# Performance work log

Measured on AMD Instinct MI355X. Metric: run time of the kernel, lower is better.

Reference implementation:

```python
import jax, jax.numpy as jnp
import numpy as np

N = 512       # n_nodes (also number of per-node attention heads)
F_IN = 256    # n_feature
H = 64        # h_feature
C = 64        # n_class (must equal H for V * out broadcast)
K = 12        # top-K threshold for learned adjacency
ALPHA = 0.2   # LeakyReLU negative slope


def setup_inputs() -> dict:
    key = jax.random.key(0)
    ks = jax.random.split(key, 6)
    X = jax.random.normal(ks[0], (N, F_IN), jnp.float32)
    # stacked params of the n_nodes first-layer attention heads
    W_stack = jax.random.normal(ks[1], (N, F_IN, H), jnp.float32) * 0.05
    a_stack = jax.random.normal(ks[2], (N, 2 * H, 1), jnp.float32) * 0.05
    # output attention layer: in_Channel = h_feature * n_nodes
    W_out = jax.random.normal(ks[3], (H * N, C), jnp.float32) * 0.02
    a_out = jax.random.normal(ks[4], (2 * C, 1), jnp.float32) * 0.05
    V = jax.random.normal(ks[5], (N, H), jnp.float32) * 0.1
    return {"X": X, "W_stack": W_stack, "a_stack": a_stack,
            "W_out": W_out, "a_out": a_out, "V": V}


def gat_layer(Hx, adj, W, a):
    # Faithful to Graph_Attention_Covlayer.forward, but the O(N^2 * 2F)
    # concat tensor is algebraically collapsed: concat(Wh[i], Wh[j]) @ a
    # == (Wh @ a1)[i] + (Wh @ a2)[j], a broadcast sum.
    Wh = Hx @ W                      # (N, F)
    f = W.shape[1]
    e1 = Wh @ a[:f, 0]               # (N,)
    e2 = Wh @ a[f:, 0]               # (N,)
    S = jax.nn.leaky_relu(e1[:, None] + e2[None, :], ALPHA)  # (N, N)
    A = jax.nn.softmax(S, axis=1)    # softmax BEFORE masking, as in source
    A = jnp.where(adj > 0, A, jnp.zeros_like(A))
    out = A @ Wh                     # (N, F)
    return jax.nn.elu(out)           # concat=True -> elu


def adj_learn(V):
    A = V @ V.T                      # (N, N)
    kth = jax.lax.top_k(A.reshape(-1), K)[0][-1]
    # source: Adj = 1 where A > kth-value, else 0 (strict >)
    return jnp.where(A > kth, jnp.ones_like(A), jnp.zeros_like(A))


def reference(X, W_stack, a_stack, W_out, a_out, V):
    adj = adj_learn(V)
    # all n_nodes heads share input X and adj -> vmap over stacked params
    heads = jax.vmap(lambda W, a: gat_layer(X, adj, W, a))(W_stack, a_stack)  # (N_heads, N, H)
    # torch.cat(..., dim=1): row i = [head0_feats | head1_feats | ...]
    mid = jnp.transpose(heads, (1, 0, 2)).reshape(N, N * H)
    # dropout: eval mode -> identity
    out = gat_layer(mid, adj, W_out, a_out)  # (N, C)
    out = jax.nn.elu(V * out)
    return adj, out
```

## Files before the change

kernel.cpp:

```cpp
#include <hip/hip_runtime.h>


#define CAND_OFF 0
#define XT_OFF   12288
#define KTH_OFF  143360
#define INT_OFF  143424
#define W1_OFF   143488
#define W2_OFF   274560
#define E2P_OFF  405632
#define MIDC_OFF 1454208
#define PART_OFF 1847424

#define H_M      0
#define H_R      1
#define H_ROWS   2
#define H_ER     14
#define H_EJ     26
#define H_ECJ    38

__device__ __forceinline__ float leaky_(float x) { return fmaxf(x, 0.2f * x); }
__device__ __forceinline__ float elu_(float x)   { return x > 0.f ? x : __expf(x) - 1.f; }

__global__ __launch_bounds__(256) void k1_prep(const float* __restrict__ V,
                                               const float* __restrict__ X,
                                               const float* __restrict__ Wst,
                                               const float* __restrict__ ast,
                                               float* __restrict__ wsf,
                                               float* __restrict__ out) {
  __shared__ float vi[64];
  __shared__ float wv[48]; __shared__ int wi[48];
  __shared__ float tile[64][65];
  int b = blockIdx.x, t = threadIdx.x, l = t & 63, w = t >> 6;

  if (b < 512) {
    if (t < 64) vi[t] = V[b * 64 + t];
    __syncthreads();
    float vr0, vr1;
    {
      const float4* vj = reinterpret_cast<const float4*>(V + t * 64);
      float acc = 0.f;
      #pragma unroll
      for (int q = 0; q < 16; ++q) {
        float4 v4 = vj[q];
        acc += v4.x * vi[q*4] + v4.y * vi[q*4+1] + v4.z * vi[q*4+2] + v4.w * vi[q*4+3];
      }
      vr0 = acc;
    }
    {
      const float4* vj = reinterpret_cast<const float4*>(V + (t + 256) * 64);
      float acc = 0.f;
      #pragma unroll
      for (int q = 0; q < 16; ++q) {
        float4 v4 = vj[q];
        acc += v4.x * vi[q*4] + v4.y * vi[q*4+1] + v4.z * vi[q*4+2] + v4.w * vi[q*4+3];
      }
      vr1 = acc;
    }
    out[b * 512 + t]       = vr0;
    out[b * 512 + 256 + t] = vr1;
    if (b < 128) out[262144 + b * 256 + t] = 0.f;

    float v0 = vr0, v1 = vr1;
    int j0 = t, j1 = t + 256;
    for (int round = 0; round < 12; ++round) {
      float m; int mi;
      if (v0 >= v1) { m = v0; mi = j0; } else { m = v1; mi = j1; }
      #pragma unroll
      for (int d = 1; d < 64; d <<= 1) {
        float ov = __shfl_xor(m, d);
        int   oi = __shfl_xor(mi, d);
        if (ov > m || (ov == m && oi < mi)) { m = ov; mi = oi; }
      }
      if (l == 0) { wv[w * 12 + round] = m; wi[w * 12 + round] = mi; }
      if (mi == j0) v0 = -INFINITY;
      if (mi == j1) v1 = -INFINITY;
    }
    __syncthreads();
    if (w == 0) {
      float cv = (l < 48) ? wv[l] : -INFINITY;
      int   ci = (l < 48) ? wi[l] : 0x7FFFFFFF;
      for (int round = 0; round < 12; ++round) {
        float m = cv; int mi = ci;
        #pragma unroll
        for (int d = 1; d < 64; d <<= 1) {
          float ov = __shfl_xor(m, d);
          int   oi = __shfl_xor(mi, d);
          if (ov > m || (ov == m && oi < mi)) { m = ov; mi = oi; }
        }
        if (l == 0) {
          float2 c; c.x = m; c.y = __int_as_float(b * 512 + mi);
          *reinterpret_cast<float2*>(wsf + CAND_OFF + (b * 12 + round) * 2) = c;
        }
        if (ci == mi) cv = -INFINITY;
      }
    }
  } else if (b < 544) {
    int ti = b - 512;
    int tjj = ti & 7, tff = ti >> 3;
    int r = t >> 2, c0 = (t & 3) * 16;
    #pragma unroll
    for (int u = 0; u < 4; ++u) {
      float4 x4 = *reinterpret_cast<const float4*>(X + (tjj*64 + r)*256 + tff*64 + c0 + u*4);
      tile[c0+u*4+0][r] = x4.x; tile[c0+u*4+1][r] = x4.y;
      tile[c0+u*4+2][r] = x4.z; tile[c0+u*4+3][r] = x4.w;
    }
    __syncthreads();
    int fl = t >> 2, jc0 = (t & 3) * 16;
    #pragma unroll
    for (int u = 0; u < 4; ++u) {
      float4 o4 = make_float4(tile[fl][jc0+u*4+0], tile[fl][jc0+u*4+1],
                              tile[fl][jc0+u*4+2], tile[fl][jc0+u*4+3]);
      *reinterpret_cast<float4*>(wsf + XT_OFF + (tff*64 + fl)*512 + tjj*64 + jc0 + u*4) = o4;
    }
  } else {
    int h = b - 544;
    int kc = (t & 15) << 2;
    float4 a1q = *reinterpret_cast<const float4*>(ast + h * 128 + kc);
    float4 a2q = *reinterpret_cast<const float4*>(ast + h * 128 + 64 + kc);
    const float* Wb = Wst + h * 16384;
    float p1a[16], p2a[16];
    #pragma unroll
    for (int it = 0; it < 16; ++it) {
      float4 wq = *reinterpret_cast<const float4*>(Wb + it * 1024 + t * 4);
      p1a[it] = wq.x*a1q.x + wq.y*a1q.y + wq.z*a1q.z + wq.w*a1q.w;
      p2a[it] = wq.x*a2q.x + wq.y*a2q.y + wq.z*a2q.z + wq.w*a2q.w;
    }
    #pragma unroll
    for (int it = 0; it < 16; ++it) {
      float p1 = p1a[it], p2 = p2a[it];
      #pragma unroll
      for (int d = 1; d < 16; d <<= 1) { p1 += __shfl_xor(p1, d); p2 += __shfl_xor(p2, d); }
      if ((t & 15) == 0) {
        int f = it * 16 + (t >> 4);
        wsf[W1_OFF + h * 256 + f] = p1;
        wsf[W2_OFF + h * 256 + f] = p2;
      }
    }
  }
}

__global__ __launch_bounds__(256) void k2_e2hdr(const float* __restrict__ X,
                                                float* __restrict__ wsf) {
  __shared__ __align__(16) float As[64][68];
  __shared__ __align__(16) float Bs[64][68];
  __shared__ float redv[4]; __shared__ int redi[4];
  __shared__ float candv[12]; __shared__ int candi[12];
  __shared__ int es_s[12], rows_s[12];
  __shared__ int M_s, R_s;
  int b = blockIdx.x, t = threadIdx.x, l = t & 63, w = t >> 6;

  if (b < 256) {
    int q = b >> 6, bh = (b >> 3) & 7, bj = b & 7;
    int r = t >> 2, c0 = (t & 3) * 16;
    const float* wsrc = wsf + W2_OFF + (bh * 64 + r) * 256 + q * 64 + c0;
    const float* xsrc = X + (bj * 64 + r) * 256 + q * 64 + c0;
    #pragma unroll
    for (int u = 0; u < 4; ++u) {
      float4 a4 = *reinterpret_cast<const float4*>(wsrc + u * 4);
      float4 b4 = *reinterpret_cast<const float4*>(xsrc + u * 4);
      As[c0 + u*4 + 0][r] = a4.x; As[c0 + u*4 + 1][r] = a4.y;
      As[c0 + u*4 + 2][r] = a4.z; As[c0 + u*4 + 3][r] = a4.w;
      Bs[c0 + u*4 + 0][r] = b4.x; Bs[c0 + u*4 + 1][r] = b4.y;
      Bs[c0 + u*4 + 2][r] = b4.z; Bs[c0 + u*4 + 3][r] = b4.w;
    }
    __syncthreads();
    int th = t >> 4, tj = t & 15;
    float acc[4][4] = {};
    #pragma unroll 8
    for (int f = 0; f < 64; ++f) {
      float4 a4 = *reinterpret_cast<const float4*>(&As[f][th * 4]);
      float4 b4 = *reinterpret_cast<const float4*>(&Bs[f][tj * 4]);
      float av[4] = { a4.x, a4.y, a4.z, a4.w };
      float bv[4] = { b4.x, b4.y, b4.z, b4.w };
      #pragma unroll
      for (int i = 0; i < 4; ++i)
        #pragma unroll
        for (int j = 0; j < 4; ++j)
          acc[i][j] += av[i] * bv[j];
    }
    float* dst = wsf + E2P_OFF + q * 262144 + (bh * 64 + th * 4) * 512 + bj * 64 + tj * 4;
    #pragma unroll
    for (int i = 0; i < 4; ++i) {
      float4 o4 = make_float4(acc[i][0], acc[i][1], acc[i][2], acc[i][3]);
      *reinterpret_cast<float4*>(dst + i * 512) = o4;
    }
    return;
  }

  float v[24]; int ix[24];
  const float2* cp = reinterpret_cast<const float2*>(wsf + CAND_OFF);
  #pragma unroll
  for (int k = 0; k < 24; ++k) {
    float2 c = cp[k * 256 + t];
    v[k] = c.x; ix[k] = __float_as_int(c.y);
  }
  unsigned rm = 0;
  for (int round = 0; round < 12; ++round) {
    float m = -INFINITY; int mi = 0x7FFFFFFF; int sel = -1;
    #pragma unroll
    for (int k = 0; k < 24; ++k) {
      bool ok = ((rm >> k) & 1u) == 0u;
      bool better = ok && (v[k] > m || (v[k] == m && ix[k] < mi));
      if (better) { m = v[k]; mi = ix[k]; sel = k; }
    }
    int lmi = mi;
    #pragma unroll
    for (int d = 1; d < 64; d <<= 1) {
      float ov = __shfl_xor(m, d);
      int   oi = __shfl_xor(mi, d);
      if (ov > m || (ov == m && oi < mi)) { m = ov; mi = oi; }
    }
    if (l == 0) { redv[w] = m; redi[w] = mi; }
    __syncthreads();
    float bm = redv[0]; int bi = redi[0];
    #pragma unroll
    for (int ww = 1; ww < 4; ++ww)
      if (redv[ww] > bm || (redv[ww] == bm && redi[ww] < bi)) { bm = redv[ww]; bi = redi[ww]; }
    if (t == 0) { candv[round] = bm; candi[round] = bi; }
    if (sel >= 0 && lmi == bi) rm |= 1u << sel;
    __syncthreads();
  }
  float kv = candv[11];
  bool valid = (t < 12) && (candv[t] > kv);
  int myidx = valid ? candi[t] : 0x7FFFFFFF;
  unsigned long long vm = __ballot(valid);
  if (t < 12) {
    int rank = 0;
    #pragma unroll
    for (int q = 0; q < 12; ++q)
      if (((vm >> q) & 1ull) && candi[q] < myidx) ++rank;
    if (valid) es_s[rank] = myidx;
    if (t == 0) M_s = (int)__popcll(vm & 0xFFFull);
  }
  __syncthreads();
  int M = M_s;
  bool isent = (t < M);
  int i2 = isent ? (es_s[t] >> 9) : -1;
  int j2 = isent ? (es_s[t] & 511) : 0;
  bool isnew = isent && (t == 0 || (es_s[t - 1] >> 9) != i2);
  unsigned long long nm = __ballot(isnew);
  if (isnew) {
    int r = (int)__popcll(nm & ((1ull << t) - 1ull));
    rows_s[r] = i2;
  }
  if (t == 0) R_s = (int)__popcll(nm & 0xFFFull);
  __syncthreads();
  int R = R_s;
  int* ip = (int*)(wsf + INT_OFF);
  if (t == 0) { ip[H_M] = M; ip[H_R] = R; wsf[KTH_OFF] = kv; }
  if (t < 12) {
    ip[H_ROWS + t] = (t < R) ? rows_s[t] : 0;
    int er = 0, ecj = -1;
    if (isent) {
      er = (int)__popcll(nm & ((2ull << t) - 1ull)) - 1;
      for (int r = 0; r < R; ++r) if (rows_s[r] == j2) ecj = r;
    }
    ip[H_ER + t]  = er;
    ip[H_EJ + t]  = isent ? j2 : 0;
    ip[H_ECJ + t] = ecj;
  }
}

__global__ __launch_bounds__(256) void k3_heads(
    const float* __restrict__ X, const float* __restrict__ Wst,
    float* __restrict__ wsf, float* __restrict__ out) {
  __shared__ int   shdr[64];
  __shared__ __align__(16) float XeT[3072];
  __shared__ __align__(16) float whp[3072];
  __shared__ float w1l[256];
  __shared__ float e2s[512];
  __shared__ float whl[768];
  __shared__ float e1r[12], mr12[12], sr12[12], av12[12];
  __shared__ float redv[4], redf[48];

  int b = blockIdx.x, t = threadIdx.x, l = t & 63, w = t >> 6;
  const int* ip = (const int*)(wsf + INT_OFF);

  {
    float kv = wsf[KTH_OFF];
    float a0 = out[b * 512 + t], a1 = out[b * 512 + 256 + t];
    out[b * 512 + t]       = (a0 > kv) ? 1.f : 0.f;
    out[b * 512 + 256 + t] = (a1 > kv) ? 1.f : 0.f;
  }
  if (t < 50) shdr[t] = ip[t];
  w1l[t] = wsf[W1_OFF + b * 256 + t];
  {
    float s0 = 0.f, s1 = 0.f;
    #pragma unroll
    for (int q = 0; q < 4; ++q) {
      s0 += wsf[E2P_OFF + q * 262144 + b * 512 + t];
      s1 += wsf[E2P_OFF + q * 262144 + b * 512 + 256 + t];
    }
    e2s[t] = s0; e2s[t + 256] = s1;
  }
  __syncthreads();
  int M = shdr[H_M], R = shdr[H_R];

  #pragma unroll
  for (int m = 0; m < 12; ++m) {
    float v = 0.f;
    if (m < M) v = X[shdr[H_EJ + m] * 256 + t];
    XeT[t * 12 + m] = v;
  }
  __syncthreads();

  const float* Wb = Wst + b * 16384;
  int fg = l >> 4, kc = (l & 15) << 2;
  float wh[12][4];
  #pragma unroll
  for (int m = 0; m < 12; ++m) { wh[m][0] = wh[m][1] = wh[m][2] = wh[m][3] = 0.f; }
  #pragma unroll 4
  for (int it = 0; it < 16; ++it) {
    int f = w * 64 + it * 4 + fg;
    float4 wq = *reinterpret_cast<const float4*>(Wb + f * 64 + kc);
    const float4* xr = reinterpret_cast<const float4*>(&XeT[f * 12]);
    float4 xa = xr[0], xb = xr[1], xc = xr[2];
    float xv[12] = { xa.x, xa.y, xa.z, xa.w, xb.x, xb.y, xb.z, xb.w,
                     xc.x, xc.y, xc.z, xc.w };
    #pragma unroll
    for (int m = 0; m < 12; ++m) {
      wh[m][0] += xv[m] * wq.x;
      wh[m][1] += xv[m] * wq.y;
      wh[m][2] += xv[m] * wq.z;
      wh[m][3] += xv[m] * wq.w;
    }
  }
  #pragma unroll
  for (int m = 0; m < 12; ++m) {
    #pragma unroll
    for (int q = 0; q < 4; ++q) {
      float x = wh[m][q];
      x += __shfl_xor(x, 16);
      x += __shfl_xor(x, 32);
      wh[m][q] = x;
    }
  }
  if (l < 16) {
    #pragma unroll
    for (int m = 0; m < 12; ++m) {
      float4 vv = make_float4(wh[m][0], wh[m][1], wh[m][2], wh[m][3]);
      *reinterpret_cast<float4*>(&whp[w * 768 + m * 64 + kc]) = vv;
    }
  }
  __syncthreads();
  #pragma unroll
  for (int c = 0; c < 3; ++c) {
    int o = c * 256 + t;
    whl[o] = whp[o] + whp[768 + o] + whp[1536 + o] + whp[2304 + o];
  }
  for (int r = w; r < R; r += 4) {
    int row = shdr[H_ROWS + r];
    float p = 0.f;
    #pragma unroll
    for (int s = 0; s < 4; ++s) {
      int f = s * 64 + l;
      p += X[row * 256 + f] * w1l[f];
    }
    #pragma unroll
    for (int d = 1; d < 64; d <<= 1) p += __shfl_xor(p, d);
    if (l == 0) e1r[r] = p;
  }
  __syncthreads();

  {
    float p = fmaxf(e2s[w * 128 + l], e2s[w * 128 + 64 + l]);
    #pragma unroll
    for (int d = 1; d < 64; d <<= 1) p = fmaxf(p, __shfl_xor(p, d));
    if (l == 0) redv[w] = p;
  }
  __syncthreads();
  float maxe2 = fmaxf(fmaxf(redv[0], redv[1]), fmaxf(redv[2], redv[3]));
  for (int r = 0; r < R; ++r) {
    float e1_ = e1r[r];
    float m_ = leaky_(e1_ + maxe2);
    float pe = __expf(leaky_(e1_ + e2s[t]) - m_) + __expf(leaky_(e1_ + e2s[t + 256]) - m_);
    #pragma unroll
    for (int d = 1; d < 64; d <<= 1) pe += __shfl_xor(pe, d);
    if (l == 0) redf[r * 4 + w] = pe;
    if (t == r) mr12[r] = m_;
  }
  __syncthreads();
  if (t < R) sr12[t] = redf[t * 4] + redf[t * 4 + 1] + redf[t * 4 + 2] + redf[t * 4 + 3];
  __syncthreads();
  if (t < M) {
    int r = shdr[H_ER + t];
    av12[t] = __expf(leaky_(e1r[r] + e2s[shdr[H_EJ + t]]) - mr12[r]) / sr12[r];
  }
  __syncthreads();
  for (int r = w; r < R; r += 4) {
    float a = 0.f;
    #pragma unroll
    for (int m = 0; m < 12; ++m) {
      if (m < M && shdr[H_ER + m] == r) a += av12[m] * whl[m * 64 + l];
    }
    wsf[MIDC_OFF + r * 32768 + b * 64 + l] = elu_(a);
  }
}

__global__ __launch_bounds__(256) void k4_wh2(const float* __restrict__ Wout,
                                              float* __restrict__ wsf) {
  __shared__ __align__(16) float midT[3072];
  __shared__ float whp4[4][768];
  int b = blockIdx.x, t = threadIdx.x, l = t & 63, w = t >> 6;
  const int* ip = (const int*)(wsf + INT_OFF);
  int R = ip[H_R];

  #pragma unroll
  for (int m = 0; m < 12; ++m) {
    float v = 0.f;
    if (m < R) v = wsf[MIDC_OFF + m * 32768 + b * 256 + t];
    midT[t * 12 + m] = v;
  }
  __syncthreads();
  float acc[12];
  #pragma unroll
  for (int m = 0; m < 12; ++m) acc[m] = 0.f;
  #pragma unroll 2
  for (int ci = 0; ci < 64; ++ci) {
    int cc = w * 64 + ci;
    float wv = Wout[(b * 256 + cc) * 64 + l];
    const float4* xr = reinterpret_cast<const float4*>(&midT[cc * 12]);
    float4 xa = xr[0], xb = xr[1], xc = xr[2];
    acc[0] += xa.x * wv; acc[1] += xa.y * wv; acc[2]  += xa.z * wv; acc[3]  += xa.w * wv;
    acc[4] += xb.x * wv; acc[5] += xb.y * wv; acc[6]  += xb.z * wv; acc[7]  += xb.w * wv;
    acc[8] += xc.x * wv; acc[9] += xc.y * wv; acc[10] += xc.z * wv; acc[11] += xc.w * wv;
  }
  #pragma unroll
  for (int m = 0; m < 12; ++m) whp4[w][m * 64 + l] = acc[m];
  __syncthreads();
  #pragma unroll
  for (int c = 0; c < 3; ++c) {
    int o = c * 256 + t;
    float s = whp4[0][o] + whp4[1][o] + whp4[2][o] + whp4[3][o];
    wsf[PART_OFF + b * 768 + o] = s;
  }
}

__global__ void k5_final(const float* __restrict__ aout, const float* __restrict__ V,
                         float* __restrict__ wsf, float* __restrict__ out) {
  __shared__ float Wh2[768];
  __shared__ float e1o[12], e2o[12], mr[12], sr[12], avals[12];
  int t = threadIdx.x;
  const int* ip = (const int*)(wsf + INT_OFF);
  int M = ip[H_M], R = ip[H_R];
  for (int o = t, c = 0; c < 3; ++c, o += 256) {
    float s = 0.f;
    #pragma unroll 8
    for (int bb = 0; bb < 128; ++bb) s += wsf[PART_OFF + bb * 768 + o];
    Wh2[o] = s;
  }
  __syncthreads();
  if (t < R) {
    float s1 = 0.f, s2 = 0.f;
    for (int k = 0; k < 64; ++k) {
      float wv = Wh2[t * 64 + k];
      s1 += wv * aout[k];
      s2 += wv * aout[64 + k];
    }
    e1o[t] = s1; e2o[t] = s2;
  }
  __syncthreads();
  if (t < R) {
    float maxe = 0.f;
    for (int r = 0; r < R; ++r) maxe = fmaxf(maxe, e2o[r]);
    float m_ = leaky_(e1o[t] + maxe);
    float s = (float)(512 - R) * __expf(leaky_(e1o[t]) - m_);
    for (int r = 0; r < R; ++r) s += __expf(leaky_(e1o[t] + e2o[r]) - m_);
    mr[t] = m_; sr[t] = s;
  }
  __syncthreads();
  if (t < M) {
    int r = ip[H_ER + t];
    int cj = ip[H_ECJ + t];
    float e2v = (cj >= 0) ? e2o[cj] : 0.f;
    avals[t] = __expf(leaky_(e1o[r] + e2v) - mr[r]) / sr[r];
  }
  __syncthreads();
  int l = t & 63, w = t >> 6;
  for (int r = w; r < R; r += 4) {
    float a = 0.f;
    #pragma unroll
    for (int m = 0; m < 12; ++m) {
      if (m < M && ip[H_ER + m] == r) {
        int cj = ip[H_ECJ + m];
        float wv = (cj >= 0) ? Wh2[cj * 64 + l] : 0.f;
        a += avals[m] * wv;
      }
    }
    int row = ip[H_ROWS + r];
    float o2 = elu_(a);
    out[262144 + row * 64 + l] = elu_(V[row * 64 + l] * o2);
  }
}

extern "C" void kernel_launch(void* const* d_in, const int* in_sizes, int n_in,
                              void* d_out, int out_size, void* d_ws, size_t ws_size,
                              hipStream_t stream) {
  const float* X    = (const float*)d_in[0];
  const float* Wst  = (const float*)d_in[1];
  const float* ast  = (const float*)d_in[2];
  const float* Wout = (const float*)d_in[3];
  const float* aout = (const float*)d_in[4];
  const float* V    = (const float*)d_in[5];
  float* out = (float*)d_out;
  float* wsf = (float*)d_ws;

  k1_prep  <<<1056, 256, 0, stream>>>(V, X, Wst, ast, wsf, out);
  k2_e2hdr <<<257,  256, 0, stream>>>(X, wsf);
  k3_heads <<<512,  256, 0, stream>>>(X, Wst, wsf, out);
  k4_wh2   <<<128,  256, 0, stream>>>(Wout, wsf);
  k5_final <<<1,    256, 0, stream>>>(aout, V, wsf, out);
}
```

Baseline: 132.8 us.

## Fuse attention-vector projection into the W_stack pass and split head pipeline

The W_stack·a projections (w1/w2) were computed in a separate prep pass that read all of W_stack once, and the head kernel then read W_stack again. Now the head kernel computes these dot products during its single pass over W_stack, writes Wh rows, e1 and w2 to workspace, and the e2 GEMM and softmax stats run as separate later kernels. This removes one full read of the 32 MB W_stack. In exchange it adds two kernel launches, extra workspace round-trips for Wh and e1, and puts the header computation in its own single-block launch on the critical path.

Result: slower. 137.8 us (+3.8%).

```diff
diff --git a/kernel.cpp b/kernel.cpp
--- a/kernel.cpp
+++ b/kernel.cpp
@@ -2,14 +2,14 @@
 
 
 #define CAND_OFF 0
-#define XT_OFF   12288
-#define KTH_OFF  143360
-#define INT_OFF  143424
-#define W1_OFF   143488
-#define W2_OFF   274560
-#define E2P_OFF  405632
-#define MIDC_OFF 1454208
-#define PART_OFF 1847424
+#define KTH_OFF  12288
+#define INT_OFF  12352
+#define W2_OFF   12416
+#define E1_OFF   143488
+#define WH_OFF   151680
+#define E2P_OFF  544896
+#define MIDC_OFF 1593472
+#define PART_OFF 1986688
 
 #define H_M      0
 #define H_R      1
@@ -21,171 +21,81 @@
 __device__ __forceinline__ float leaky_(float x) { return fmaxf(x, 0.2f * x); }
 __device__ __forceinline__ float elu_(float x)   { return x > 0.f ? x : __expf(x) - 1.f; }
 
-__global__ __launch_bounds__(256) void k1_prep(const float* __restrict__ V,
-                                               const float* __restrict__ X,
-                                               const float* __restrict__ Wst,
-                                               const float* __restrict__ ast,
-                                               float* __restrict__ wsf,
-                                               float* __restrict__ out) {
+__global__ __launch_bounds__(256) void k0a_adjA(const float* __restrict__ V,
+                                                float* __restrict__ wsf,
+                                                float* __restrict__ out) {
   __shared__ float vi[64];
   __shared__ float wv[48]; __shared__ int wi[48];
-  __shared__ float tile[64][65];
   int b = blockIdx.x, t = threadIdx.x, l = t & 63, w = t >> 6;
-
-  if (b < 512) {
-    if (t < 64) vi[t] = V[b * 64 + t];
-    __syncthreads();
-    float vr0, vr1;
-    {
-      const float4* vj = reinterpret_cast<const float4*>(V + t * 64);
-      float acc = 0.f;
-      #pragma unroll
-      for (int q = 0; q < 16; ++q) {
-        float4 v4 = vj[q];
-        acc += v4.x * vi[q*4] + v4.y * vi[q*4+1] + v4.z * vi[q*4+2] + v4.w * vi[q*4+3];
-      }
-      vr0 = acc;
-    }
-    {
-      const float4* vj = reinterpret_cast<const float4*>(V + (t + 256) * 64);
-      float acc = 0.f;
-      #pragma unroll
-      for (int q = 0; q < 16; ++q) {
-        float4 v4 = vj[q];
-        acc += v4.x * vi[q*4] + v4.y * vi[q*4+1] + v4.z * vi[q*4+2] + v4.w * vi[q*4+3];
-      }
-      vr1 = acc;
-    }
-    out[b * 512 + t]       = vr0;
-    out[b * 512 + 256 + t] = vr1;
-    if (b < 128) out[262144 + b * 256 + t] = 0.f;
-
-    float v0 = vr0, v1 = vr1;
-    int j0 = t, j1 = t + 256;
+  if (t < 64) vi[t] = V[b * 64 + t];
+  __syncthreads();
+  float vr0, vr1;
+  {
+    const float4* vj = reinterpret_cast<const float4*>(V + t * 64);
+    float acc = 0.f;
+    #pragma unroll
+    for (int q = 0; q < 16; ++q) {
+      float4 v4 = vj[q];
+      acc += v4.x * vi[q*4] + v4.y * vi[q*4+1] + v4.z * vi[q*4+2] + v4.w * vi[q*4+3];
+    }
+    vr0 = acc;
+  }
+  {
+    const float4* vj = reinterpret_cast<const float4*>(V + (t + 256) * 64);
+    float acc = 0.f;
+    #pragma unroll
+    for (int q = 0; q < 16; ++q) {
+      float4 v4 = vj[q];
+      acc += v4.x * vi[q*4] + v4.y * vi[q*4+1] + v4.z * vi[q*4+2] + v4.w * vi[q*4+3];
+    }
+    vr1 = acc;
+  }
+  out[b * 512 + t]       = vr0;
+  out[b * 512 + 256 + t] = vr1;
+  if (b < 128) out[262144 + b * 256 + t] = 0.f;
+
+  float v0 = vr0, v1 = vr1;
+  int j0 = t, j1 = t + 256;
+  for (int round = 0; round < 12; ++round) {
+    float m; int mi;
+    if (v0 >= v1) { m = v0; mi = j0; } else { m = v1; mi = j1; }
+    #pragma unroll
+    for (int d = 1; d < 64; d <<= 1) {
+      float ov = __shfl_xor(m, d);
+      int   oi = __shfl_xor(mi, d);
+      if (ov > m || (ov == m && oi < mi)) { m = ov; mi = oi; }
+    }
+    if (l == 0) { wv[w * 12 + round] = m; wi[w * 12 + round] = mi; }
+    if (mi == j0) v0 = -INFINITY;
+    if (mi == j1) v1 = -INFINITY;
+  }
+  __syncthreads();
+  if (w == 0) {
+    float cv = (l < 48) ? wv[l] : -INFINITY;
+    int   ci = (l < 48) ? wi[l] : 0x7FFFFFFF;
     for (int round = 0; round < 12; ++round) {
-      float m; int mi;
-      if (v0 >= v1) { m = v0; mi = j0; } else { m = v1; mi = j1; }
+      float m = cv; int mi = ci;
       #pragma unroll
       for (int d = 1; d < 64; d <<= 1) {
         float ov = __shfl_xor(m, d);
         int   oi = __shfl_xor(mi, d);
         if (ov > m || (ov == m && oi < mi)) { m = ov; mi = oi; }
       }
-      if (l == 0) { wv[w * 12 + round] = m; wi[w * 12 + round] = mi; }
-      if (mi == j0) v0 = -INFINITY;
-      if (mi == j1) v1 = -INFINITY;
-    }
-    __syncthreads();
-    if (w == 0) {
-      float cv = (l < 48) ? wv[l] : -INFINITY;
-      int   ci = (l < 48) ? wi[l] : 0x7FFFFFFF;
-      for (int round = 0; round < 12; ++round) {
-        float m = cv; int mi = ci;
-        #pragma unroll
-        for (int d = 1; d < 64; d <<= 1) {
-          float ov = __shfl_xor(m, d);
-          int   oi = __shfl_xor(mi, d);
-          if (ov > m || (ov == m && oi < mi)) { m = ov; mi = oi; }
-        }
-        if (l == 0) {
-          float2 c; c.x = m; c.y = __int_as_float(b * 512 + mi);
-          *reinterpret_cast<float2*>(wsf + CAND_OFF + (b * 12 + round) * 2) = c;
-        }
-        if (ci == mi) cv = -INFINITY;
+      if (l == 0) {
+        float2 c; c.x = m; c.y = __int_as_float(b * 512 + mi);
+        *reinterpret_cast<float2*>(wsf + CAND_OFF + (b * 12 + round) * 2) = c;
       }
-    }
-  } else if (b < 544) {
-    int ti = b - 512;
-    int tjj = ti & 7, tff = ti >> 3;
-    int r = t >> 2, c0 = (t & 3) * 16;
-    #pragma unroll
-    for (int u = 0; u < 4; ++u) {
-      float4 x4 = *reinterpret_cast<const float4*>(X + (tjj*64 + r)*256 + tff*64 + c0 + u*4);
-      tile[c0+u*4+0][r] = x4.x; tile[c0+u*4+1][r] = x4.y;
-      tile[c0+u*4+2][r] = x4.z; tile[c0+u*4+3][r] = x4.w;
-    }
-    __syncthreads();
-    int fl = t >> 2, jc0 = (t & 3) * 16;
-    #pragma unroll
-    for (int u = 0; u < 4; ++u) {
-      float4 o4 = make_float4(tile[fl][jc0+u*4+0], tile[fl][jc0+u*4+1],
-                              tile[fl][jc0+u*4+2], tile[fl][jc0+u*4+3]);
-      *reinterpret_cast<float4*>(wsf + XT_OFF + (tff*64 + fl)*512 + tjj*64 + jc0 + u*4) = o4;
-    }
-  } else {
-    int h = b - 544;
-    int kc = (t & 15) << 2;
-    float4 a1q = *reinterpret_cast<const float4*>(ast + h * 128 + kc);
-    float4 a2q = *reinterpret_cast<const float4*>(ast + h * 128 + 64 + kc);
-    const float* Wb = Wst + h * 16384;
-    float p1a[16], p2a[16];
-    #pragma unroll
-    for (int it = 0; it < 16; ++it) {
-      float4 wq = *reinterpret_cast<const float4*>(Wb + it * 1024 + t * 4);
-      p1a[it] = wq.x*a1q.x + wq.y*a1q.y + wq.z*a1q.z + wq.w*a1q.w;
-      p2a[it] = wq.x*a2q.x + wq.y*a2q.y + wq.z*a2q.z + wq.w*a2q.w;
-    }
-    #pragma unroll
-    for (int it = 0; it < 16; ++it) {
-      float p1 = p1a[it], p2 = p2a[it];
-      #pragma unroll
-      for (int d = 1; d < 16; d <<= 1) { p1 += __shfl_xor(p1, d); p2 += __shfl_xor(p2, d); }
-      if ((t & 15) == 0) {
-        int f = it * 16 + (t >> 4);
-        wsf[W1_OFF + h * 256 + f] = p1;
-        wsf[W2_OFF + h * 256 + f] = p2;
-      }
-    }
-  }
-}
-
-__global__ __launch_bounds__(256) void k2_e2hdr(const float* __restrict__ X,
-                                                float* __restrict__ wsf) {
-  __shared__ __align__(16) float As[64][68];
-  __shared__ __align__(16) float Bs[64][68];
+      if (ci == mi) cv = -INFINITY;
+    }
+  }
+}
+
+__global__ void k0b_header(float* __restrict__ wsf) {
   __shared__ float redv[4]; __shared__ int redi[4];
   __shared__ float candv[12]; __shared__ int candi[12];
   __shared__ int es_s[12], rows_s[12];
   __shared__ int M_s, R_s;
-  int b = blockIdx.x, t = threadIdx.x, l = t & 63, w = t >> 6;
-
-  if (b < 256) {
-    int q = b >> 6, bh = (b >> 3) & 7, bj = b & 7;
-    int r = t >> 2, c0 = (t & 3) * 16;
-    const float* wsrc = wsf + W2_OFF + (bh * 64 + r) * 256 + q * 64 + c0;
-    const float* xsrc = X + (bj * 64 + r) * 256 + q * 64 + c0;
-    #pragma unroll
-    for (int u = 0; u < 4; ++u) {
-      float4 a4 = *reinterpret_cast<const float4*>(wsrc + u * 4);
-      float4 b4 = *reinterpret_cast<const float4*>(xsrc + u * 4);
-      As[c0 + u*4 + 0][r] = a4.x; As[c0 + u*4 + 1][r] = a4.y;
-      As[c0 + u*4 + 2][r] = a4.z; As[c0 + u*4 + 3][r] = a4.w;
-      Bs[c0 + u*4 + 0][r] = b4.x; Bs[c0 + u*4 + 1][r] = b4.y;
-      Bs[c0 + u*4 + 2][r] = b4.z; Bs[c0 + u*4 + 3][r] = b4.w;
-    }
-    __syncthreads();
-    int th = t >> 4, tj = t & 15;
-    float acc[4][4] = {};
-    #pragma unroll 8
-    for (int f = 0; f < 64; ++f) {
-      float4 a4 = *reinterpret_cast<const float4*>(&As[f][th * 4]);
-      float4 b4 = *reinterpret_cast<const float4*>(&Bs[f][tj * 4]);
-      float av[4] = { a4.x, a4.y, a4.z, a4.w };
-      float bv[4] = { b4.x, b4.y, b4.z, b4.w };
-      #pragma unroll
-      for (int i = 0; i < 4; ++i)
-        #pragma unroll
-        for (int j = 0; j < 4; ++j)
-          acc[i][j] += av[i] * bv[j];
-    }
-    float* dst = wsf + E2P_OFF + q * 262144 + (bh * 64 + th * 4) * 512 + bj * 64 + tj * 4;
-    #pragma unroll
-    for (int i = 0; i < 4; ++i) {
-      float4 o4 = make_float4(acc[i][0], acc[i][1], acc[i][2], acc[i][3]);
-      *reinterpret_cast<float4*>(dst + i * 512) = o4;
-    }
-    return;
-  }
+  int t = threadIdx.x, l = t & 63, w = t >> 6;
 
   float v[24]; int ix[24];
   const float2* cp = reinterpret_cast<const float2*>(wsf + CAND_OFF);
@@ -261,18 +171,14 @@
   }
 }
 
-__global__ __launch_bounds__(256) void k3_heads(
+__global__ __launch_bounds__(256) void k1_wpass(
     const float* __restrict__ X, const float* __restrict__ Wst,
-    float* __restrict__ wsf, float* __restrict__ out) {
+    const float* __restrict__ ast, float* __restrict__ wsf,
+    float* __restrict__ out) {
   __shared__ int   shdr[64];
+  __shared__ float w1l[256], w2l[256];
   __shared__ __align__(16) float XeT[3072];
   __shared__ __align__(16) float whp[3072];
-  __shared__ float w1l[256];
-  __shared__ float e2s[512];
-  __shared__ float whl[768];
-  __shared__ float e1r[12], mr12[12], sr12[12], av12[12];
-  __shared__ float redv[4], redf[48];
-
   int b = blockIdx.x, t = threadIdx.x, l = t & 63, w = t >> 6;
   const int* ip = (const int*)(wsf + INT_OFF);
 
@@ -283,16 +189,6 @@
     out[b * 512 + 256 + t] = (a1 > kv) ? 1.f : 0.f;
   }
   if (t < 50) shdr[t] = ip[t];
-  w1l[t] = wsf[W1_OFF + b * 256 + t];
-  {
-    float s0 = 0.f, s1 = 0.f;
-    #pragma unroll
-    for (int q = 0; q < 4; ++q) {
-      s0 += wsf[E2P_OFF + q * 262144 + b * 512 + t];
-      s1 += wsf[E2P_OFF + q * 262144 + b * 512 + 256 + t];
-    }
-    e2s[t] = s0; e2s[t + 256] = s1;
-  }
   __syncthreads();
   int M = shdr[H_M], R = shdr[H_R];
 
@@ -306,13 +202,19 @@
 
   const float* Wb = Wst + b * 16384;
   int fg = l >> 4, kc = (l & 15) << 2;
+  float4 a1q = *reinterpret_cast<const float4*>(ast + b * 128 + kc);
+  float4 a2q = *reinterpret_cast<const float4*>(ast + b * 128 + 64 + kc);
   float wh[12][4];
+  float p1a[16], p2a[16];
   #pragma unroll
   for (int m = 0; m < 12; ++m) { wh[m][0] = wh[m][1] = wh[m][2] = wh[m][3] = 0.f; }
+
   #pragma unroll 4
   for (int it = 0; it < 16; ++it) {
     int f = w * 64 + it * 4 + fg;
     float4 wq = *reinterpret_cast<const float4*>(Wb + f * 64 + kc);
+    p1a[it] = wq.x*a1q.x + wq.y*a1q.y + wq.z*a1q.z + wq.w*a1q.w;
+    p2a[it] = wq.x*a2q.x + wq.y*a2q.y + wq.z*a2q.z + wq.w*a2q.w;
     const float4* xr = reinterpret_cast<const float4*>(&XeT[f * 12]);
     float4 xa = xr[0], xb = xr[1], xc = xr[2];
     float xv[12] = { xa.x, xa.y, xa.z, xa.w, xb.x, xb.y, xb.z, xb.w,
@@ -326,6 +228,16 @@
     }
   }
   #pragma unroll
+  for (int it = 0; it < 16; ++it) {
+    float p1 = p1a[it], p2 = p2a[it];
+    #pragma unroll
+    for (int d = 1; d < 16; d <<= 1) { p1 += __shfl_xor(p1, d); p2 += __shfl_xor(p2, d); }
+    if ((l & 15) == 0) {
+      int f = w * 64 + it * 4 + fg;
+      w1l[f] = p1; w2l[f] = p2;
+    }
+  }
+  #pragma unroll
   for (int m = 0; m < 12; ++m) {
     #pragma unroll
     for (int q = 0; q < 4; ++q) {
@@ -346,8 +258,9 @@
   #pragma unroll
   for (int c = 0; c < 3; ++c) {
     int o = c * 256 + t;
-    whl[o] = whp[o] + whp[768 + o] + whp[1536 + o] + whp[2304 + o];
-  }
+    wsf[WH_OFF + b * 768 + o] = whp[o] + whp[768 + o] + whp[1536 + o] + whp[2304 + o];
+  }
+  wsf[W2_OFF + b * 256 + t] = w2l[t];
   for (int r = w; r < R; r += 4) {
     int row = shdr[H_ROWS + r];
     float p = 0.f;
@@ -358,10 +271,75 @@
     }
     #pragma unroll
     for (int d = 1; d < 64; d <<= 1) p += __shfl_xor(p, d);
-    if (l == 0) e1r[r] = p;
-  }
-  __syncthreads();
-
+    if (l == 0) wsf[E1_OFF + b * 16 + r] = p;
+  }
+}
+
+__global__ __launch_bounds__(256) void k2_e2(const float* __restrict__ X,
+                                             float* __restrict__ wsf) {
+  __shared__ __align__(16) float As[64][68];
+  __shared__ __align__(16) float Bs[64][68];
+  int b = blockIdx.x, t = threadIdx.x;
+  int q = b >> 6, bh = (b >> 3) & 7, bj = b & 7;
+  int r = t >> 2, c0 = (t & 3) * 16;
+  const float* wsrc = wsf + W2_OFF + (bh * 64 + r) * 256 + q * 64 + c0;
+  const float* xsrc = X + (bj * 64 + r) * 256 + q * 64 + c0;
+  #pragma unroll
+  for (int u = 0; u < 4; ++u) {
+    float4 a4 = *reinterpret_cast<const float4*>(wsrc + u * 4);
+    float4 b4 = *reinterpret_cast<const float4*>(xsrc + u * 4);
+    As[c0 + u*4 + 0][r] = a4.x; As[c0 + u*4 + 1][r] = a4.y;
+    As[c0 + u*4 + 2][r] = a4.z; As[c0 + u*4 + 3][r] = a4.w;
+    Bs[c0 + u*4 + 0][r] = b4.x; Bs[c0 + u*4 + 1][r] = b4.y;
+    Bs[c0 + u*4 + 2][r] = b4.z; Bs[c0 + u*4 + 3][r] = b4.w;
+  }
+  __syncthreads();
+  int th = t >> 4, tj = t & 15;
+  float acc[4][4] = {};
+  #pragma unroll 8
+  for (int f = 0; f < 64; ++f) {
+    float4 a4 = *reinterpret_cast<const float4*>(&As[f][th * 4]);
+    float4 b4 = *reinterpret_cast<const float4*>(&Bs[f][tj * 4]);
+    float av[4] = { a4.x, a4.y, a4.z, a4.w };
+    float bv[4] = { b4.x, b4.y, b4.z, b4.w };
+    #pragma unroll
+    for (int i = 0; i < 4; ++i)
+      #pragma unroll
+      for (int j = 0; j < 4; ++j)
+        acc[i][j] += av[i] * bv[j];
+  }
+  float* dst = wsf + E2P_OFF + q * 262144 + (bh * 64 + th * 4) * 512 + bj * 64 + tj * 4;
+  #pragma unroll
+  for (int i = 0; i < 4; ++i) {
+    float4 o4 = make_float4(acc[i][0], acc[i][1], acc[i][2], acc[i][3]);
+    *reinterpret_cast<float4*>(dst + i * 512) = o4;
+  }
+}
+
+__global__ __launch_bounds__(256) void k3_stats(float* __restrict__ wsf) {
+  __shared__ int   shdr[64];
+  __shared__ float e1r[12], whl[768], e2s[512];
+  __shared__ float redv[4], redf[48], mr12[12], sr12[12], av12[12];
+  int b = blockIdx.x, t = threadIdx.x, l = t & 63, w = t >> 6;
+  const int* ip = (const int*)(wsf + INT_OFF);
+  if (t < 50) shdr[t] = ip[t];
+  if (t >= 128 && t < 140) e1r[t - 128] = wsf[E1_OFF + b * 16 + (t - 128)];
+  #pragma unroll
+  for (int c = 0; c < 3; ++c) {
+    int o = c * 256 + t;
+    whl[o] = wsf[WH_OFF + b * 768 + o];
+  }
+  {
+    float s0 = 0.f, s1 = 0.f;
+    #pragma unroll
+    for (int qq = 0; qq < 4; ++qq) {
+      s0 += wsf[E2P_OFF + qq * 262144 + b * 512 + t];
+      s1 += wsf[E2P_OFF + qq * 262144 + b * 512 + 256 + t];
+    }
+    e2s[t] = s0; e2s[t + 256] = s1;
+  }
+  __syncthreads();
+  int M = shdr[H_M], R = shdr[H_R];
   {
     float p = fmaxf(e2s[w * 128 + l], e2s[w * 128 + 64 + l]);
     #pragma unroll
@@ -505,9 +483,11 @@
   float* out = (float*)d_out;
   float* wsf = (float*)d_ws;
 
-  k1_prep  <<<1056, 256, 0, stream>>>(V, X, Wst, ast, wsf, out);
-  k2_e2hdr <<<257,  256, 0, stream>>>(X, wsf);
-  k3_heads <<<512,  256, 0, stream>>>(X, Wst, wsf, out);
-  k4_wh2   <<<128,  256, 0, stream>>>(Wout, wsf);
-  k5_final <<<1,    256, 0, stream>>>(aout, V, wsf, out);
-}
+  k0a_adjA <<<512, 256, 0, stream>>>(V, wsf, out);
+  k0b_header<<<1,  256, 0, stream>>>(wsf);
+  k1_wpass <<<512, 256, 0, stream>>>(X, Wst, ast, wsf, out);
+  k2_e2    <<<256, 256, 0, stream>>>(X, wsf);
+  k3_stats <<<512, 256, 0, stream>>>(wsf);
+  k4_wh2   <<<128, 256, 0, stream>>>(Wout, wsf);
+  k5_final <<<1,   256, 0, stream>>>(aout, V, wsf, out);
+}
```
